# Performance work log

Hardware: AMD Instinct MI355X
Metric: run time of the kernel (lower is better)

## Reference

```python
import jax, jax.numpy as jnp
import numpy as np

NUM_GROUPS = 32
EPS = 1e-4
N_HEADS = 8


def group_norm(x, w, b):
    # x: [B, C, L]; normalize over (channels-in-group, L)
    bsz, c, l = x.shape
    xg = x.reshape(bsz, NUM_GROUPS, c // NUM_GROUPS, l)
    mu = jnp.mean(xg, axis=(2, 3), keepdims=True)
    var = jnp.var(xg, axis=(2, 3), keepdims=True)
    xn = ((xg - mu) * jax.lax.rsqrt(var + EPS)).reshape(bsz, c, l)
    return xn * w[None, :, None] + b[None, :, None]


def setup_inputs() -> dict:
    key = jax.random.key(0)
    ks = jax.random.split(key, 7)
    B, C, H, W = 16, 512, 32, 32
    return {
        "x": jax.random.normal(ks[0], (B, C, H, W), dtype=jnp.float32),
        "norm_w": jax.random.uniform(ks[1], (C,), dtype=jnp.float32, minval=0.5, maxval=1.5),
        "norm_b": jax.random.normal(ks[2], (C,), dtype=jnp.float32) * 0.1,
        "qkv_w": jax.random.normal(ks[3], (3 * C, C), dtype=jnp.float32) * (1.0 / np.sqrt(C)),
        "qkv_b": jax.random.normal(ks[4], (3 * C,), dtype=jnp.float32) * 0.02,
        "proj_w": jax.random.normal(ks[5], (C, C), dtype=jnp.float32) * (1.0 / np.sqrt(C)),
        "proj_b": jax.random.normal(ks[6], (C,), dtype=jnp.float32) * 0.02,
    }


def reference(x, norm_w, norm_b, qkv_w, qkv_b, proj_w, proj_b):
    b, c, hh, ww = x.shape
    l = hh * ww
    xf = x.reshape(b, c, l)
    # GroupNorm + 1x1 conv (pointwise) -> qkv: [B, 3C, L]
    qkv = jnp.einsum('oc,bcl->bol', qkv_w, group_norm(xf, norm_w, norm_b)) + qkv_b[None, :, None]
    ch = c // N_HEADS
    q, k, v = jnp.split(qkv, 3, axis=1)
    q = q.reshape(b * N_HEADS, ch, l)
    k = k.reshape(b * N_HEADS, ch, l)
    v = v.reshape(b * N_HEADS, ch, l)
    scale = ch ** -0.25
    # full O(L^2) attention matrix, as in OldQKVAttention
    weight = jnp.einsum('bct,bcs->bts', q * scale, k * scale)
    weight = jax.nn.softmax(weight, axis=-1)
    a = jnp.einsum('bts,bcs->bct', weight, v).reshape(b, c, l)
    h = jnp.einsum('oc,bcl->bol', proj_w, a) + proj_b[None, :, None]
    return (xf + h).reshape(b, c, hh, ww)
```

## Files before the change

kernel.cpp:

```cpp
#include <hip/hip_runtime.h>
#include <cmath>


#define BATCH 16
#define CDIM 512
#define LDIM 1024
#define NX (8388608u)
#define NQ (786432u)
#define NP (262144u)

typedef unsigned short u16;
typedef u16 ushort8v __attribute__((ext_vector_type(8)));
typedef __bf16 bf16x8_t __attribute__((ext_vector_type(8)));
typedef float f32x4 __attribute__((ext_vector_type(4)));

__device__ __forceinline__ u16 f2bf(float f) {
  unsigned u = __float_as_uint(f);
  unsigned r = u + 0x7fffu + ((u >> 16) & 1u);
  return (u16)(r >> 16);
}
__device__ __forceinline__ unsigned pack2(float a, float b) {
  return (unsigned)f2bf(a) | ((unsigned)f2bf(b) << 16);
}
__device__ __forceinline__ unsigned pack2t(float a, float b) {
  return __builtin_amdgcn_perm(__float_as_uint(b), __float_as_uint(a), 0x07060302u);
}
__device__ __forceinline__ float bftrunc(float x) {
  return __uint_as_float(__float_as_uint(x) & 0xffff0000u);
}
__device__ __forceinline__ float fast_exp2(float x) {
#if __has_builtin(__builtin_amdgcn_exp2f)
  return __builtin_amdgcn_exp2f(x);
#else
  return exp2f(x);
#endif
}
__device__ __forceinline__ f32x4 mfma16(ushort8v a, ushort8v b, f32x4 c) {
  return __builtin_amdgcn_mfma_f32_16x16x32_bf16(
      __builtin_bit_cast(bf16x8_t, a), __builtin_bit_cast(bf16x8_t, b), c, 0, 0, 0);
}

__global__ __launch_bounds__(256) void gn_stats_kernel(const float* __restrict__ x,
                                                       const float* __restrict__ w,
                                                       const float* __restrict__ bvec,
                                                       float* __restrict__ scl,
                                                       float* __restrict__ sh) {
  int bg = blockIdx.x;
  int bb = bg >> 5, g = bg & 31;
  size_t base = ((size_t)bb * CDIM + g * 16) * LDIM;
  const float4* x4 = (const float4*)(x + base);
  int tid = threadIdx.x;
  float sum = 0.f, ss = 0.f;
#pragma unroll
  for (int i = 0; i < 16; ++i) {
    float4 v = x4[tid + 256 * i];
    sum += v.x + v.y + v.z + v.w;
    ss += v.x * v.x + v.y * v.y + v.z * v.z + v.w * v.w;
  }
#pragma unroll
  for (int off = 32; off; off >>= 1) {
    sum += __shfl_xor(sum, off);
    ss += __shfl_xor(ss, off);
  }
  __shared__ float rs[4], rq[4];
  int lane = tid & 63, wv = tid >> 6;
  if (lane == 0) { rs[wv] = sum; rq[wv] = ss; }
  __syncthreads();
  sum = rs[0] + rs[1] + rs[2] + rs[3];
  ss = rq[0] + rq[1] + rq[2] + rq[3];
  const float inv_n = 1.f / (16.f * 1024.f);
  float mean = sum * inv_n;
  float var = ss * inv_n - mean * mean;
  float rstd = rsqrtf(var + 1e-4f);
  if (tid < 16) {
    int c = g * 16 + tid;
    float s = w[c] * rstd;
    scl[bb * CDIM + c] = s;
    sh[bb * CDIM + c] = bvec[c] - mean * s;
  }
}

__global__ __launch_bounds__(256) void prep_kernel(const float* __restrict__ x,
                                                   const float* __restrict__ scl,
                                                   const float* __restrict__ sh,
                                                   const float* __restrict__ wq,
                                                   const float* __restrict__ wp,
                                                   u16* __restrict__ xn,
                                                   u16* __restrict__ wqb,
                                                   u16* __restrict__ wpb) {
  size_t i = (size_t)blockIdx.x * 2048 + (size_t)threadIdx.x * 8;
  float s_ = 1.f, h_ = 0.f;
  const float* sp;
  u16* dp;
  size_t off;
  if (i < NX) {
    off = i;
    sp = x;
    dp = xn;
    size_t bc = i >> 10;
    s_ = scl[bc];
    h_ = sh[bc];
  } else if (i < NX + NQ) {
    off = i - NX;
    sp = wq;
    dp = wqb;
  } else {
    off = i - NX - NQ;
    sp = wp;
    dp = wpb;
  }
  float4 a = *(const float4*)&sp[off];
  float4 b = *(const float4*)&sp[off + 4];
  uint4 o;
  o.x = pack2(a.x * s_ + h_, a.y * s_ + h_);
  o.y = pack2(a.z * s_ + h_, a.w * s_ + h_);
  o.z = pack2(b.x * s_ + h_, b.y * s_ + h_);
  o.w = pack2(b.z * s_ + h_, b.w * s_ + h_);
  *(uint4*)&dp[off] = o;
}

template <int MODE>
__global__ __launch_bounds__(256) void gemm_mfma(
    const u16* __restrict__ Wb, const float* __restrict__ biasg,
    const u16* __restrict__ Xb, const float* __restrict__ resid,
    u16* __restrict__ qo, u16* __restrict__ ko,
    u16* __restrict__ vo, float* __restrict__ fo) {
  __shared__ __align__(16) u16 Ws[128][40];
  __shared__ __align__(16) u16 Xs[128][40];
  int bb = blockIdx.z;
  int m0 = blockIdx.y * 128;
  int n0 = blockIdx.x * 128;
  int tid = threadIdx.x;
  int w = tid >> 6, lane = tid & 63, quad = lane >> 4, l15 = lane & 15;
  int wm = (w >> 1) * 64, wn = (w & 1) * 64;
  f32x4 acc[4][4] = {};
  int xkb = tid >> 5, xnb = tid & 31;
  bool qkpath = (MODE == 0) && (m0 < 1024);

  for (int kk = 0; kk < 512; kk += 32) {
    uint4 aw[2];
#pragma unroll
    for (int r = 0; r < 2; ++r) {
      int f = tid + 256 * r;
      aw[r] = *(const uint4*)&Wb[(size_t)(m0 + (f >> 2)) * 512 + kk + (f & 3) * 8];
    }
    ushort4 xu[4];
#pragma unroll
    for (int r = 0; r < 4; ++r)
      xu[r] = *(const ushort4*)&Xb[((size_t)bb * CDIM + kk + xkb * 4 + r) * LDIM + n0 + xnb * 4];
    uint2 xw[4];
#pragma unroll
    for (int j = 0; j < 4; ++j) {
      const u16* p0 = (const u16*)&xu[0];
      const u16* p1 = (const u16*)&xu[1];
      const u16* p2 = (const u16*)&xu[2];
      const u16* p3 = (const u16*)&xu[3];
      xw[j].x = (unsigned)p0[j] | ((unsigned)p1[j] << 16);
      xw[j].y = (unsigned)p2[j] | ((unsigned)p3[j] << 16);
    }
    __syncthreads();
#pragma unroll
    for (int r = 0; r < 2; ++r) {
      int f = tid + 256 * r;
      *(uint4*)&Ws[f >> 2][(f & 3) * 8] = aw[r];
    }
#pragma unroll
    for (int j = 0; j < 4; ++j) *(uint2*)&Xs[xnb * 4 + j][xkb * 4] = xw[j];
    __syncthreads();
    ushort8v af[4], bfr[4];
#pragma unroll
    for (int i = 0; i < 4; ++i) af[i] = *(const ushort8v*)&Ws[wm + i * 16 + l15][quad * 8];
#pragma unroll
    for (int i = 0; i < 4; ++i) bfr[i] = *(const ushort8v*)&Xs[wn + i * 16 + l15][quad * 8];
    if (qkpath) {
#pragma unroll
      for (int i = 0; i < 4; ++i)
#pragma unroll
        for (int j = 0; j < 4; ++j) acc[j][i] = mfma16(bfr[j], af[i], acc[j][i]);
    } else {
#pragma unroll
      for (int i = 0; i < 4; ++i)
#pragma unroll
        for (int j = 0; j < 4; ++j) acc[i][j] = mfma16(af[i], bfr[j], acc[i][j]);
    }
  }

  if (MODE == 0 && m0 < 1024) {
    bool isQ = (m0 < 512);
    float qscale = isQ ? (0.125f * 1.44269504f) : 1.0f;
    u16* dst = isQ ? qo : ko;
    int cbase0 = m0 - (isQ ? 0 : 512) + wm;
#pragma unroll
    for (int i = 0; i < 4; ++i) {
      int cg = cbase0 + i * 16 + l15;
      float bv = biasg[m0 + wm + i * 16 + l15];
      int hh = cg >> 6, cl = cg & 63;
      size_t rowbase = ((size_t)(bb * 8 + hh) * 1024) * 64 + cl;
#pragma unroll
      for (int j = 0; j < 4; ++j)
#pragma unroll
        for (int r = 0; r < 4; ++r) {
          int t = n0 + wn + j * 16 + quad * 4 + r;
          dst[rowbase + (size_t)t * 64] = f2bf((acc[j][i][r] + bv) * qscale);
        }
    }
  } else if (MODE == 0) {
#pragma unroll
    for (int i = 0; i < 4; ++i)
#pragma unroll
      for (int r = 0; r < 4; ++r) {
        int m_abs = m0 + wm + i * 16 + quad * 4 + r;
        float bv = biasg[m_abs];
        int cg = m_abs - 1024;
#pragma unroll
        for (int j = 0; j < 4; ++j) {
          int n = n0 + wn + j * 16 + l15;
          vo[((size_t)bb * CDIM + cg) * LDIM + n] = f2bf(acc[i][j][r] + bv);
        }
      }
  } else {
#pragma unroll
    for (int i = 0; i < 4; ++i)
#pragma unroll
      for (int r = 0; r < 4; ++r) {
        int m_abs = m0 + wm + i * 16 + quad * 4 + r;
        float bv = biasg[m_abs];
#pragma unroll
        for (int j = 0; j < 4; ++j) {
          int n = n0 + wn + j * 16 + l15;
          size_t off = ((size_t)bb * CDIM + m_abs) * LDIM + n;
          fo[off] = acc[i][j][r] + bv + resid[off];
        }
      }
  }
}

__global__ __launch_bounds__(256) void attn_mfma(const u16* __restrict__ qt,
                                                 const u16* __restrict__ kt,
                                                 const u16* __restrict__ vv,
                                                 u16* __restrict__ av_out) {
  __shared__ __align__(16) u16 Ks[2][32][72];
  __shared__ __align__(16) u16 Vs[2][64][40];
  __shared__ __align__(16) u16 Ps[4][32][40];
  int bh = blockIdx.x;
  int t0b = blockIdx.y * 128;
  int b = bh >> 3, h = bh & 7;
  int tid = threadIdx.x;
  int w = tid >> 6, lane = tid & 63, quad = lane >> 4, l15 = lane & 15;
  int t0w = t0b + w * 32;
  size_t head = (size_t)bh * 65536;
  const u16* kbase = kt + head;
  const u16* vbase = vv + head;

  int sK = tid >> 3, cK8 = (tid & 7) * 8;
  int cV = tid >> 2, sV8 = (tid & 3) * 8;

  ushort8v qf[2][2];
#pragma unroll
  for (int ts = 0; ts < 2; ++ts)
#pragma unroll
    for (int kc = 0; kc < 2; ++kc)
      qf[ts][kc] =
          *(const ushort8v*)&qt[head + (size_t)(t0w + ts * 16 + l15) * 64 + kc * 32 + quad * 8];

  f32x4 Co[4][2] = {};
  float lacc[2] = {0.f, 0.f};

  {
    uint4 k0 = *(const uint4*)&kbase[(size_t)tid * 8];
    uint4 v0 = *(const uint4*)&vbase[(size_t)cV * 1024 + sV8];
    *(uint4*)&Ks[0][sK][cK8] = k0;
    *(uint4*)&Vs[0][cV][sV8] = v0;
  }
  __syncthreads();

  int cur = 0;
  for (int ci = 0; ci < 32; ++ci) {
    int sn = ((ci + 1) & 31) * 32;
    uint4 kn = *(const uint4*)&kbase[(size_t)sn * 64 + tid * 8];
    uint4 vn = *(const uint4*)&vbase[(size_t)cV * 1024 + sn + sV8];

    ushort8v kf[2][2];
#pragma unroll
    for (int ms = 0; ms < 2; ++ms)
#pragma unroll
      for (int kc = 0; kc < 2; ++kc)
        kf[ms][kc] = *(const ushort8v*)&Ks[cur][ms * 16 + l15][kc * 32 + quad * 8];
    ushort8v vf[4];
#pragma unroll
    for (int cs = 0; cs < 4; ++cs) vf[cs] = *(const ushort8v*)&Vs[cur][cs * 16 + l15][quad * 8];

    f32x4 st[2][2];
#pragma unroll
    for (int ts = 0; ts < 2; ++ts)
#pragma unroll
      for (int ms = 0; ms < 2; ++ms) {
        f32x4 z = {};
        z = mfma16(kf[ms][0], qf[ts][0], z);
        st[ts][ms] = mfma16(kf[ms][1], qf[ts][1], z);
      }
#pragma unroll
    for (int ts = 0; ts < 2; ++ts) {
      float p0 = fast_exp2(st[ts][0].x), p1 = fast_exp2(st[ts][0].y);
      float p2 = fast_exp2(st[ts][0].z), p3 = fast_exp2(st[ts][0].w);
      float p4 = fast_exp2(st[ts][1].x), p5 = fast_exp2(st[ts][1].y);
      float p6 = fast_exp2(st[ts][1].z), p7 = fast_exp2(st[ts][1].w);
      lacc[ts] += ((bftrunc(p0) + bftrunc(p1)) + (bftrunc(p2) + bftrunc(p3))) +
                  ((bftrunc(p4) + bftrunc(p5)) + (bftrunc(p6) + bftrunc(p7)));
      uint2 u0, u1;
      u0.x = pack2t(p0, p1);
      u0.y = pack2t(p2, p3);
      u1.x = pack2t(p4, p5);
      u1.y = pack2t(p6, p7);
      *(uint2*)&Ps[w][ts * 16 + l15][quad * 4] = u0;
      *(uint2*)&Ps[w][ts * 16 + l15][16 + quad * 4] = u1;
    }
    ushort8v pb[2];
#pragma unroll
    for (int ts = 0; ts < 2; ++ts) pb[ts] = *(const ushort8v*)&Ps[w][ts * 16 + l15][quad * 8];
#pragma unroll
    for (int cs = 0; cs < 4; ++cs)
#pragma unroll
      for (int ts = 0; ts < 2; ++ts) Co[cs][ts] = mfma16(vf[cs], pb[ts], Co[cs][ts]);

    int nxt = cur ^ 1;
    *(uint4*)&Ks[nxt][sK][cK8] = kn;
    *(uint4*)&Vs[nxt][cV][sV8] = vn;
    __syncthreads();
    cur = nxt;
  }

#pragma unroll
  for (int ts = 0; ts < 2; ++ts) {
    lacc[ts] += __shfl_xor(lacc[ts], 16);
    lacc[ts] += __shfl_xor(lacc[ts], 32);
  }
  float inv[2] = {1.f / lacc[0], 1.f / lacc[1]};
#pragma unroll
  for (int cs = 0; cs < 4; ++cs)
#pragma unroll
    for (int ts = 0; ts < 2; ++ts) {
      int t = t0w + ts * 16 + l15;
#pragma unroll
      for (int r = 0; r < 4; ++r) {
        int c = h * 64 + cs * 16 + quad * 4 + r;
        av_out[((size_t)b * CDIM + c) * LDIM + t] = f2bf(Co[cs][ts][r] * inv[ts]);
      }
    }
}

extern "C" void kernel_launch(void* const* d_in, const int* in_sizes, int n_in,
                              void* d_out, int out_size, void* d_ws, size_t ws_size,
                              hipStream_t stream) {
  const float* x = (const float*)d_in[0];
  const float* norm_w = (const float*)d_in[1];
  const float* norm_b = (const float*)d_in[2];
  const float* qkv_w = (const float*)d_in[3];
  const float* qkv_b = (const float*)d_in[4];
  const float* proj_w = (const float*)d_in[5];
  const float* proj_b = (const float*)d_in[6];
  float* out = (float*)d_out;

  const size_t NE = (size_t)BATCH * CDIM * LDIM;
  float* scl = (float*)d_ws;
  float* sh = scl + BATCH * CDIM;
  u16* qt = (u16*)(sh + BATCH * CDIM);
  u16* kt = qt + NE;
  u16* vv = kt + NE;
  u16* av = vv + NE;
  u16* xn = av + NE;
  u16* wqb = xn + NE;
  u16* wpb = wqb + NQ;

  gn_stats_kernel<<<dim3(BATCH * 32), dim3(256), 0, stream>>>(x, norm_w, norm_b, scl, sh);
  prep_kernel<<<dim3((NX + NQ + NP) / 2048), dim3(256), 0, stream>>>(
      x, scl, sh, qkv_w, proj_w, xn, wqb, wpb);
  gemm_mfma<0><<<dim3(8, 12, BATCH), dim3(256), 0, stream>>>(
      wqb, qkv_b, xn, (const float*)nullptr, qt, kt, vv, (float*)nullptr);
  attn_mfma<<<dim3(128, 8), dim3(256), 0, stream>>>(qt, kt, vv, av);
  gemm_mfma<2><<<dim3(8, 4, BATCH), dim3(256), 0, stream>>>(
      wpb, proj_b, av, x, (u16*)nullptr, (u16*)nullptr, (u16*)nullptr, out);
}
```

Baseline: 256.9 us.

## Store activations channel-last and stage GEMM tiles with direct global-to-LDS loads

GroupNorm-applied activations and the attention output are now written in [B, L, C] layout. A new transpose kernel handles the normalized input, and the attention epilogue writes transposed, using a small LDS table of per-row reciprocals. With both GEMM operands K-contiguous, the GEMM can stage tiles with `__builtin_amdgcn_global_load_lds` (16-byte DMA into unpadded LDS) instead of register loads plus an in-register transpose. This removes VGPR staging and shuffle work but also drops the load/compute overlap the register prefetch gave. It adds a trailing barrier, and the unpadded 32-wide LDS rows may cause bank conflicts. Weight packing is split into its own kernel.

```diff
diff --git a/kernel.cpp b/kernel.cpp
--- a/kernel.cpp
+++ b/kernel.cpp
@@ -5,9 +5,11 @@
 #define BATCH 16
 #define CDIM 512
 #define LDIM 1024
-#define NX (8388608u)
 #define NQ (786432u)
 #define NP (262144u)
+
+#define AS1 __attribute__((address_space(1)))
+#define AS3 __attribute__((address_space(3)))
 
 typedef unsigned short u16;
 typedef u16 ushort8v __attribute__((ext_vector_type(8)));
@@ -38,6 +40,9 @@
 __device__ __forceinline__ f32x4 mfma16(ushort8v a, ushort8v b, f32x4 c) {
   return __builtin_amdgcn_mfma_f32_16x16x32_bf16(
       __builtin_bit_cast(bf16x8_t, a), __builtin_bit_cast(bf16x8_t, b), c, 0, 0, 0);
+}
+__device__ __forceinline__ void g2l16(const u16* g, u16* l) {
+  __builtin_amdgcn_global_load_lds((const AS1 void*)g, (AS3 void*)l, 16, 0, 0);
 }
 
 __global__ __launch_bounds__(256) void gn_stats_kernel(const float* __restrict__ x,
@@ -80,98 +85,93 @@
   }
 }
 
-__global__ __launch_bounds__(256) void prep_kernel(const float* __restrict__ x,
-                                                   const float* __restrict__ scl,
-                                                   const float* __restrict__ sh,
-                                                   const float* __restrict__ wq,
-                                                   const float* __restrict__ wp,
-                                                   u16* __restrict__ xn,
-                                                   u16* __restrict__ wqb,
-                                                   u16* __restrict__ wpb) {
+__global__ __launch_bounds__(256) void wpack_kernel(const float* __restrict__ wq,
+                                                    const float* __restrict__ wp,
+                                                    u16* __restrict__ wqb,
+                                                    u16* __restrict__ wpb) {
   size_t i = (size_t)blockIdx.x * 2048 + (size_t)threadIdx.x * 8;
-  float s_ = 1.f, h_ = 0.f;
   const float* sp;
   u16* dp;
   size_t off;
-  if (i < NX) {
+  if (i < NQ) {
     off = i;
-    sp = x;
-    dp = xn;
-    size_t bc = i >> 10;
-    s_ = scl[bc];
-    h_ = sh[bc];
-  } else if (i < NX + NQ) {
-    off = i - NX;
     sp = wq;
     dp = wqb;
   } else {
-    off = i - NX - NQ;
+    off = i - NQ;
     sp = wp;
     dp = wpb;
   }
   float4 a = *(const float4*)&sp[off];
   float4 b = *(const float4*)&sp[off + 4];
   uint4 o;
-  o.x = pack2(a.x * s_ + h_, a.y * s_ + h_);
-  o.y = pack2(a.z * s_ + h_, a.w * s_ + h_);
-  o.z = pack2(b.x * s_ + h_, b.y * s_ + h_);
-  o.w = pack2(b.z * s_ + h_, b.w * s_ + h_);
+  o.x = pack2(a.x, a.y);
+  o.y = pack2(a.z, a.w);
+  o.z = pack2(b.x, b.y);
+  o.w = pack2(b.z, b.w);
   *(uint4*)&dp[off] = o;
+}
+
+__global__ __launch_bounds__(256) void xpose_kernel(const float* __restrict__ x,
+                                                    const float* __restrict__ scl,
+                                                    const float* __restrict__ sh,
+                                                    u16* __restrict__ xnT) {
+  __shared__ u16 T[64][72];
+  int b = blockIdx.z, c0 = blockIdx.y * 64, l0 = blockIdx.x * 64;
+  int tid = threadIdx.x;
+  int ci = tid >> 4, ljs = (tid & 15) * 4;
+#pragma unroll
+  for (int rep = 0; rep < 4; ++rep) {
+    int c = rep * 16 + ci;
+    float s_ = scl[b * CDIM + c0 + c];
+    float h_ = sh[b * CDIM + c0 + c];
+    float4 v = *(const float4*)&x[((size_t)b * CDIM + c0 + c) * LDIM + l0 + ljs];
+    T[ljs + 0][c] = f2bf(v.x * s_ + h_);
+    T[ljs + 1][c] = f2bf(v.y * s_ + h_);
+    T[ljs + 2][c] = f2bf(v.z * s_ + h_);
+    T[ljs + 3][c] = f2bf(v.w * s_ + h_);
+  }
+  __syncthreads();
+  int lr = tid >> 2, cs8 = (tid & 3) * 16;
+  uint4 o0 = *(const uint4*)&T[lr][cs8];
+  uint4 o1 = *(const uint4*)&T[lr][cs8 + 8];
+  size_t dst = ((size_t)b * LDIM + l0 + lr) * CDIM + c0 + cs8;
+  *(uint4*)&xnT[dst] = o0;
+  *(uint4*)&xnT[dst + 8] = o1;
 }
 
 template <int MODE>
 __global__ __launch_bounds__(256) void gemm_mfma(
     const u16* __restrict__ Wb, const float* __restrict__ biasg,
-    const u16* __restrict__ Xb, const float* __restrict__ resid,
+    const u16* __restrict__ Xt, const float* __restrict__ resid,
     u16* __restrict__ qo, u16* __restrict__ ko,
     u16* __restrict__ vo, float* __restrict__ fo) {
-  __shared__ __align__(16) u16 Ws[128][40];
-  __shared__ __align__(16) u16 Xs[128][40];
+  __shared__ __align__(16) u16 As_[128][32];
+  __shared__ __align__(16) u16 Xs_[128][32];
   int bb = blockIdx.z;
   int m0 = blockIdx.y * 128;
   int n0 = blockIdx.x * 128;
   int tid = threadIdx.x;
   int w = tid >> 6, lane = tid & 63, quad = lane >> 4, l15 = lane & 15;
   int wm = (w >> 1) * 64, wn = (w & 1) * 64;
+  int srow = lane >> 2, scol = (lane & 3) * 8;
+  const u16* Xb = Xt + (size_t)bb * LDIM * CDIM;
   f32x4 acc[4][4] = {};
-  int xkb = tid >> 5, xnb = tid & 31;
   bool qkpath = (MODE == 0) && (m0 < 1024);
 
   for (int kk = 0; kk < 512; kk += 32) {
-    uint4 aw[2];
 #pragma unroll
     for (int r = 0; r < 2; ++r) {
-      int f = tid + 256 * r;
-      aw[r] = *(const uint4*)&Wb[(size_t)(m0 + (f >> 2)) * 512 + kk + (f & 3) * 8];
-    }
-    ushort4 xu[4];
-#pragma unroll
-    for (int r = 0; r < 4; ++r)
-      xu[r] = *(const ushort4*)&Xb[((size_t)bb * CDIM + kk + xkb * 4 + r) * LDIM + n0 + xnb * 4];
-    uint2 xw[4];
-#pragma unroll
-    for (int j = 0; j < 4; ++j) {
-      const u16* p0 = (const u16*)&xu[0];
-      const u16* p1 = (const u16*)&xu[1];
-      const u16* p2 = (const u16*)&xu[2];
-      const u16* p3 = (const u16*)&xu[3];
-      xw[j].x = (unsigned)p0[j] | ((unsigned)p1[j] << 16);
-      xw[j].y = (unsigned)p2[j] | ((unsigned)p3[j] << 16);
-    }
-    __syncthreads();
-#pragma unroll
-    for (int r = 0; r < 2; ++r) {
-      int f = tid + 256 * r;
-      *(uint4*)&Ws[f >> 2][(f & 3) * 8] = aw[r];
-    }
-#pragma unroll
-    for (int j = 0; j < 4; ++j) *(uint2*)&Xs[xnb * 4 + j][xkb * 4] = xw[j];
+      int row = w * 32 + r * 16;
+      g2l16(&Wb[(size_t)(m0 + row + srow) * 512 + kk + scol], &As_[row][0]);
+      g2l16(&Xb[(size_t)(n0 + row + srow) * 512 + kk + scol], &Xs_[row][0]);
+    }
     __syncthreads();
     ushort8v af[4], bfr[4];
 #pragma unroll
-    for (int i = 0; i < 4; ++i) af[i] = *(const ushort8v*)&Ws[wm + i * 16 + l15][quad * 8];
-#pragma unroll
-    for (int i = 0; i < 4; ++i) bfr[i] = *(const ushort8v*)&Xs[wn + i * 16 + l15][quad * 8];
+    for (int i = 0; i < 4; ++i) af[i] = *(const ushort8v*)&As_[wm + i * 16 + l15][quad * 8];
+#pragma unroll
+    for (int i = 0; i < 4; ++i) bfr[i] = *(const ushort8v*)&Xs_[wn + i * 16 + l15][quad * 8];
     if (qkpath) {
 #pragma unroll
       for (int i = 0; i < 4; ++i)
@@ -183,6 +183,7 @@
 #pragma unroll
         for (int j = 0; j < 4; ++j) acc[i][j] = mfma16(af[i], bfr[j], acc[i][j]);
     }
+    __syncthreads();
   }
 
   if (MODE == 0 && m0 < 1024) {
@@ -238,10 +239,11 @@
 __global__ __launch_bounds__(256) void attn_mfma(const u16* __restrict__ qt,
                                                  const u16* __restrict__ kt,
                                                  const u16* __restrict__ vv,
-                                                 u16* __restrict__ av_out) {
+                                                 u16* __restrict__ avT) {
   __shared__ __align__(16) u16 Ks[2][32][72];
   __shared__ __align__(16) u16 Vs[2][64][40];
   __shared__ __align__(16) u16 Ps[4][32][40];
+  __shared__ float linv[4][32];
   int bh = blockIdx.x;
   int t0b = blockIdx.y * 128;
   int b = bh >> 3, h = bh & 7;
@@ -263,7 +265,7 @@
       qf[ts][kc] =
           *(const ushort8v*)&qt[head + (size_t)(t0w + ts * 16 + l15) * 64 + kc * 32 + quad * 8];
 
-  f32x4 Co[4][2] = {};
+  f32x4 Co[2][4] = {};
   float lacc[2] = {0.f, 0.f};
 
   {
@@ -319,9 +321,9 @@
 #pragma unroll
     for (int ts = 0; ts < 2; ++ts) pb[ts] = *(const ushort8v*)&Ps[w][ts * 16 + l15][quad * 8];
 #pragma unroll
-    for (int cs = 0; cs < 4; ++cs)
-#pragma unroll
-      for (int ts = 0; ts < 2; ++ts) Co[cs][ts] = mfma16(vf[cs], pb[ts], Co[cs][ts]);
+    for (int ts = 0; ts < 2; ++ts)
+#pragma unroll
+      for (int cs = 0; cs < 4; ++cs) Co[ts][cs] = mfma16(pb[ts], vf[cs], Co[ts][cs]);
 
     int nxt = cur ^ 1;
     *(uint4*)&Ks[nxt][sK][cK8] = kn;
@@ -334,18 +336,18 @@
   for (int ts = 0; ts < 2; ++ts) {
     lacc[ts] += __shfl_xor(lacc[ts], 16);
     lacc[ts] += __shfl_xor(lacc[ts], 32);
-  }
-  float inv[2] = {1.f / lacc[0], 1.f / lacc[1]};
-#pragma unroll
-  for (int cs = 0; cs < 4; ++cs)
-#pragma unroll
-    for (int ts = 0; ts < 2; ++ts) {
-      int t = t0w + ts * 16 + l15;
-#pragma unroll
-      for (int r = 0; r < 4; ++r) {
-        int c = h * 64 + cs * 16 + quad * 4 + r;
-        av_out[((size_t)b * CDIM + c) * LDIM + t] = f2bf(Co[cs][ts][r] * inv[ts]);
-      }
+    if (quad == 0) linv[w][ts * 16 + l15] = 1.f / lacc[ts];
+  }
+#pragma unroll
+  for (int ts = 0; ts < 2; ++ts)
+#pragma unroll
+    for (int r = 0; r < 4; ++r) {
+      int tl = ts * 16 + quad * 4 + r;
+      float iv = linv[w][tl];
+      size_t rowb = ((size_t)b * LDIM + t0w + tl) * CDIM + h * 64;
+#pragma unroll
+      for (int cs = 0; cs < 4; ++cs)
+        avT[rowb + cs * 16 + l15] = f2bf(Co[ts][cs][r] * iv);
     }
 }
 
@@ -373,11 +375,11 @@
   u16* wpb = wqb + NQ;
 
   gn_stats_kernel<<<dim3(BATCH * 32), dim3(256), 0, stream>>>(x, norm_w, norm_b, scl, sh);
-  prep_kernel<<<dim3((NX + NQ + NP) / 2048), dim3(256), 0, stream>>>(
-      x, scl, sh, qkv_w, proj_w, xn, wqb, wpb);
+  wpack_kernel<<<dim3((NQ + NP) / 2048), dim3(256), 0, stream>>>(qkv_w, proj_w, wqb, wpb);
+  xpose_kernel<<<dim3(16, 8, BATCH), dim3(256), 0, stream>>>(x, scl, sh, xn);
   gemm_mfma<0><<<dim3(8, 12, BATCH), dim3(256), 0, stream>>>(
       wqb, qkv_b, xn, (const float*)nullptr, qt, kt, vv, (float*)nullptr);
   attn_mfma<<<dim3(128, 8), dim3(256), 0, stream>>>(qt, kt, vv, av);
-  gemm_mfma<2><<<dim3(8, 4, BATCH), dim3(256), 0, stream>>>(
+  gemm_mfma<1><<<dim3(8, 4, BATCH), dim3(256), 0, stream>>>(
       wpb, proj_b, av, x, (u16*)nullptr, (u16*)nullptr, (u16*)nullptr, out);
 }
```

Measured after the change: 213.9 us. 16.7% less time.
